# Performance work log

Measured on AMD Instinct MI355X. Metric: run time of the kernel, lower is better.

Reference implementation:

```python
import jax, jax.numpy as jnp
import numpy as np

B, K, N, F, H = 20000, 10, 100000, 256, 128


def setup_inputs() -> dict:
    key = jax.random.key(0)
    ks = jax.random.split(key, 8)
    neighbors = jax.random.randint(ks[0], (B, K), 0, N)
    embed_table = jax.random.normal(ks[1], (N, F), dtype=jnp.float32)
    w = lambda k, shp: jax.random.normal(k, shp, dtype=jnp.float32) * 0.05
    return {
        "neighbors": neighbors,
        "embed_table": embed_table,
        "W1a": w(ks[2], (F, H)), "W1b": w(ks[3], (H, H)),
        "W2a": w(ks[4], (F, H)), "W2b": w(ks[5], (H, H)),
        "W3a": w(ks[6], (F, H)), "W3b": w(ks[7], (H, H)),
    }


def reference(neighbors, embed_table, W1a, W1b, W2a, W2b, W3a, W3b):
    # Gather each batch node's K sampled neighbor embeddings: [B, K, F]
    x = embed_table[neighbors]
    # Three MLP projections: Linear(F,H,no bias) -> tanh -> Linear(H,H,no bias)
    q = jnp.tanh(x @ W1a) @ W1b              # [B, K, H]  (att1)
    k = jnp.tanh(x @ W2a) @ W2b              # [B, K, H]  (att2)
    v = jnp.tanh(x @ W3a) @ W3b              # [B, K, H]  (att3)
    # Per-node attention over the K neighbors, softmax along last dim
    att = jax.nn.softmax(jnp.einsum('bid,bjd->bij', q, k), axis=-1)  # [B, K, K]
    # torch: sum over rows of (att @ v) -> contract both i and j
    out = jnp.einsum('bij,bjd->bd', att, v)  # [B, H]
    return out
```

## Files before the change

### kernel.cpp

```cpp
#include <hip/hip_runtime.h>
#include <hip/hip_bf16.h>

constexpr int B_ = 20000;
constexpr int K_ = 10;
constexpr int N_ = 100000;
constexpr int F_ = 256;
constexpr int H_ = 128;
constexpr int RW = 3 * H_;

typedef __attribute__((ext_vector_type(8))) short bf16x8;
typedef __attribute__((ext_vector_type(4))) float f32x4;
typedef __attribute__((ext_vector_type(4))) unsigned short ushort4v;

__device__ __forceinline__ unsigned short f2bf(float x) {
  unsigned int u = __builtin_bit_cast(unsigned int, x);
  unsigned int r = u + 0x7fffu + ((u >> 16) & 1u);
  return (unsigned short)(r >> 16);
}

__device__ __forceinline__ float bf2f(unsigned int u16) {
  return __builtin_bit_cast(float, u16 << 16);
}

__device__ __forceinline__ unsigned int cvt_pk_bf16(float lo, float hi) {
  unsigned int r;
  asm("v_cvt_pk_bf16_f32 %0, %1, %2" : "=v"(r) : "v"(lo), "v"(hi));
  return r;
}

__device__ __forceinline__ float fast_tanh(float x) {
  float e = __expf(2.0f * x);
  return 1.0f - 2.0f * __builtin_amdgcn_rcpf(e + 1.0f);
}

__global__ __launch_bounds__(256) void prep_kernel(
    const float* __restrict__ W1a, const float* __restrict__ W1b,
    const float* __restrict__ W2a, const float* __restrict__ W2b,
    const float* __restrict__ W3a, const float* __restrict__ W3b,
    unsigned short* __restrict__ wat2, unsigned short* __restrict__ wbt2) {
  const float* Wa[3] = {W1a, W2a, W3a};
  const float* Wb[3] = {W1b, W2b, W3b};
  int g = blockIdx.x * 256 + threadIdx.x;
  if (g < 3 * 64 * 512) {
    int chunk = g >> 9;
    int e = g & 511;
    int lane = e >> 3, j = e & 7;
    int c = chunk & 7;
    int ks = (chunk >> 3) & 7;
    int p = chunk >> 6;
    int k = 32 * ks + 8 * (lane >> 4) + j;
    int h = 16 * c + (lane & 15);
    wat2[g] = f2bf(Wa[p][k * H_ + h]);
  } else {
    int g2 = g - 3 * 64 * 512;
    int chunk = g2 >> 9;
    int e = g2 & 511;
    int lane = e >> 3, j = e & 7;
    int ks2 = chunk & 3;
    int c2 = (chunk >> 2) & 7;
    int p = chunk >> 5;
    int k = 32 * ks2 + 8 * (lane >> 4) + j;
    int h2 = 16 * c2 + (lane & 15);
    wbt2[g2] = f2bf(Wb[p][k * H_ + h2]);
  }
}

constexpr int MT = 32;
constexpr int XS = F_ + 8;
constexpr int TS = H_ + 8;

__global__ __launch_bounds__(256) void proj_kernel(
    const float* __restrict__ E,
    const unsigned short* __restrict__ wat2,
    const unsigned short* __restrict__ wbt2,
    unsigned short* __restrict__ qkvI) {
  __shared__ unsigned short xs[MT * XS];
  __shared__ unsigned short ts[MT * TS];

  const int tid = threadIdx.x;
  const int lane = tid & 63;
  const int w = tid >> 6;
  const int l15 = lane & 15;
  const int q = lane >> 4;
  const int row0 = blockIdx.x * MT;

  {
    const float4* Eg = (const float4*)E;
#pragma unroll
    for (int it = 0; it < 8; ++it) {
      int i = tid + 256 * it;
      int r = i >> 6;
      int c4 = i & 63;
      int row = row0 + r;
      if (row >= N_) row = N_ - 1;
      float4 v = Eg[(size_t)row * (F_ / 4) + c4];
      unsigned int lo = cvt_pk_bf16(v.x, v.y);
      unsigned int hi = cvt_pk_bf16(v.z, v.w);
      *(uint2*)&xs[r * XS + c4 * 4] = make_uint2(lo, hi);
    }
  }
  __syncthreads();

  for (int p = 0; p < 3; ++p) {
    const unsigned short* __restrict__ wa = wat2 + p * (64 * 512);
    const unsigned short* __restrict__ wb = wbt2 + p * (32 * 512);

    bf16x8 af[2][8];
#pragma unroll
    for (int ks = 0; ks < 8; ++ks) {
      af[0][ks] = *(const bf16x8*)&wa[(ks * 8 + 2 * w) * 512 + lane * 8];
      af[1][ks] = *(const bf16x8*)&wa[(ks * 8 + 2 * w + 1) * 512 + lane * 8];
    }

    f32x4 acc[2][2];
#pragma unroll
    for (int i = 0; i < 2; ++i)
#pragma unroll
      for (int j = 0; j < 2; ++j) acc[i][j] = (f32x4)0.0f;

#pragma unroll
    for (int ks = 0; ks < 8; ++ks) {
      bf16x8 bx0 = *(const bf16x8*)&xs[(l15)*XS + 32 * ks + 8 * q];
      bf16x8 bx1 = *(const bf16x8*)&xs[(16 + l15) * XS + 32 * ks + 8 * q];
      acc[0][0] = __builtin_amdgcn_mfma_f32_16x16x32_bf16(af[0][ks], bx0, acc[0][0], 0, 0, 0);
      acc[0][1] = __builtin_amdgcn_mfma_f32_16x16x32_bf16(af[0][ks], bx1, acc[0][1], 0, 0, 0);
      acc[1][0] = __builtin_amdgcn_mfma_f32_16x16x32_bf16(af[1][ks], bx0, acc[1][0], 0, 0, 0);
      acc[1][1] = __builtin_amdgcn_mfma_f32_16x16x32_bf16(af[1][ks], bx1, acc[1][1], 0, 0, 0);
    }

    bf16x8 ab[2][4];
#pragma unroll
    for (int ks2 = 0; ks2 < 4; ++ks2) {
      ab[0][ks2] = *(const bf16x8*)&wb[((2 * w) * 4 + ks2) * 512 + lane * 8];
      ab[1][ks2] = *(const bf16x8*)&wb[((2 * w + 1) * 4 + ks2) * 512 + lane * 8];
    }

    __syncthreads();
#pragma unroll
    for (int i = 0; i < 2; ++i)
#pragma unroll
      for (int j = 0; j < 2; ++j) {
        unsigned int lo = cvt_pk_bf16(fast_tanh(acc[i][j][0]), fast_tanh(acc[i][j][1]));
        unsigned int hi = cvt_pk_bf16(fast_tanh(acc[i][j][2]), fast_tanh(acc[i][j][3]));
        *(uint2*)&ts[(16 * j + l15) * TS + 16 * (2 * w + i) + 4 * q] =
            make_uint2(lo, hi);
      }
    __syncthreads();

    f32x4 ac2[2][2];
#pragma unroll
    for (int i = 0; i < 2; ++i)
#pragma unroll
      for (int j = 0; j < 2; ++j) ac2[i][j] = (f32x4)0.0f;

#pragma unroll
    for (int ks2 = 0; ks2 < 4; ++ks2) {
      bf16x8 bt0 = *(const bf16x8*)&ts[(l15)*TS + 32 * ks2 + 8 * q];
      bf16x8 bt1 = *(const bf16x8*)&ts[(16 + l15) * TS + 32 * ks2 + 8 * q];
      ac2[0][0] = __builtin_amdgcn_mfma_f32_16x16x32_bf16(ab[0][ks2], bt0, ac2[0][0], 0, 0, 0);
      ac2[0][1] = __builtin_amdgcn_mfma_f32_16x16x32_bf16(ab[0][ks2], bt1, ac2[0][1], 0, 0, 0);
      ac2[1][0] = __builtin_amdgcn_mfma_f32_16x16x32_bf16(ab[1][ks2], bt0, ac2[1][0], 0, 0, 0);
      ac2[1][1] = __builtin_amdgcn_mfma_f32_16x16x32_bf16(ab[1][ks2], bt1, ac2[1][1], 0, 0, 0);
    }

#pragma unroll
    for (int i = 0; i < 2; ++i)
#pragma unroll
      for (int j = 0; j < 2; ++j) {
        int n = row0 + 16 * j + l15;
        if (n < N_) {
          unsigned int lo = cvt_pk_bf16(ac2[i][j][0], ac2[i][j][1]);
          unsigned int hi = cvt_pk_bf16(ac2[i][j][2], ac2[i][j][3]);
          *(uint2*)&qkvI[(size_t)n * RW + p * H_ + 16 * (2 * w + i) + 4 * q] =
              make_uint2(lo, hi);
        }
      }
  }
}

__global__ __launch_bounds__(256) void agg_kernel(
    const int* __restrict__ nbr,
    const unsigned short* __restrict__ qkvI,
    float* __restrict__ out) {
  const int lane = threadIdx.x & 63;
  const int wv = threadIdx.x >> 6;
  const int b = blockIdx.x * 4 + wv;
  const int l15 = lane & 15;
  const int kg = lane >> 4;

  const int ni = nbr[b * K_ + (l15 < K_ ? l15 : 0)];
  const size_t nbase = (size_t)ni * RW;

  f32x4 sc = (f32x4)0.0f;
#pragma unroll
  for (int k = 0; k < 4; ++k) {
    const int off = k * 32 + kg * 8;
    bf16x8 qf = *(const bf16x8*)&qkvI[nbase + off];
    bf16x8 kf = *(const bf16x8*)&qkvI[nbase + H_ + off];
    sc = __builtin_amdgcn_mfma_f32_16x16x32_bf16(qf, kf, sc, 0, 0, 0);
  }

  if (l15 >= K_) {
#pragma unroll
    for (int r = 0; r < 4; ++r) sc[r] = -3.0e38f;
  }

  float mx[4], e[4], sm[4];
#pragma unroll
  for (int r = 0; r < 4; ++r) mx[r] = sc[r];
#pragma unroll
  for (int st = 1; st < 16; st <<= 1)
#pragma unroll
    for (int r = 0; r < 4; ++r) mx[r] = fmaxf(mx[r], __shfl_xor(mx[r], st, 16));
#pragma unroll
  for (int r = 0; r < 4; ++r) { e[r] = __expf(sc[r] - mx[r]); sm[r] = e[r]; }
#pragma unroll
  for (int st = 1; st < 16; st <<= 1)
#pragma unroll
    for (int r = 0; r < 4; ++r) sm[r] += __shfl_xor(sm[r], st, 16);

  float cs = 0.0f;
#pragma unroll
  for (int r = 0; r < 4; ++r) {
    float a = e[r] * __builtin_amdgcn_rcpf(sm[r]);
    if (kg * 4 + r >= K_) a = 0.0f;
    cs += a;
  }
  cs += __shfl_xor(cs, 16, 64);
  cs += __shfl_xor(cs, 32, 64);

  float o0 = 0.0f, o1 = 0.0f;
#pragma unroll
  for (int j = 0; j < K_; ++j) {
    const float cj = __shfl(cs, j, 64);
    const int nj = __shfl(ni, j, 64);
    const unsigned int v2 =
        *(const unsigned int*)&qkvI[(size_t)nj * RW + 2 * H_ + 2 * lane];
    o0 = fmaf(cj, bf2f(v2 & 0xffffu), o0);
    o1 = fmaf(cj, bf2f(v2 >> 16), o1);
  }
  *(float2*)&out[(size_t)b * H_ + 2 * lane] = make_float2(o0, o1);
}

extern "C" void kernel_launch(void* const* d_in, const int* in_sizes, int n_in,
                              void* d_out, int out_size, void* d_ws, size_t ws_size,
                              hipStream_t stream) {
  const int* nbr = (const int*)d_in[0];
  const float* E = (const float*)d_in[1];
  const float* W1a = (const float*)d_in[2];
  const float* W1b = (const float*)d_in[3];
  const float* W2a = (const float*)d_in[4];
  const float* W2b = (const float*)d_in[5];
  const float* W3a = (const float*)d_in[6];
  const float* W3b = (const float*)d_in[7];
  float* out = (float*)d_out;

  unsigned short* qkvI = (unsigned short*)d_ws;
  unsigned short* wat2 = qkvI + (size_t)N_ * RW;
  unsigned short* wbt2 = wat2 + (size_t)3 * 64 * 512;

  prep_kernel<<<(3 * 64 * 512 + 3 * 32 * 512) / 256, 256, 0, stream>>>(
      W1a, W1b, W2a, W2b, W3a, W3b, wat2, wbt2);
  proj_kernel<<<N_ / MT, 256, 0, stream>>>(E, wat2, wbt2, qkvI);
  agg_kernel<<<B_ / 4, 256, 0, stream>>>(nbr, qkvI, out);
}
```

Baseline: 236.4 us.

## Double projection row tile to 64 and split warps over H and rows

Measured after the change: 307.7 us. 1.3x slower.

```diff
diff --git a/kernel.cpp b/kernel.cpp
--- a/kernel.cpp
+++ b/kernel.cpp
@@ -10,7 +10,6 @@
 
 typedef __attribute__((ext_vector_type(8))) short bf16x8;
 typedef __attribute__((ext_vector_type(4))) float f32x4;
-typedef __attribute__((ext_vector_type(4))) unsigned short ushort4v;
 
 __device__ __forceinline__ unsigned short f2bf(float x) {
   unsigned int u = __builtin_bit_cast(unsigned int, x);
@@ -65,7 +64,7 @@
   }
 }
 
-constexpr int MT = 32;
+constexpr int MT = 64;
 constexpr int XS = F_ + 8;
 constexpr int TS = H_ + 8;
 
@@ -80,6 +79,8 @@
   const int tid = threadIdx.x;
   const int lane = tid & 63;
   const int w = tid >> 6;
+  const int wh = w >> 1;
+  const int wn = w & 1;
   const int l15 = lane & 15;
   const int q = lane >> 4;
   const int row0 = blockIdx.x * MT;
@@ -87,7 +88,7 @@
   {
     const float4* Eg = (const float4*)E;
 #pragma unroll
-    for (int it = 0; it < 8; ++it) {
+    for (int it = 0; it < 16; ++it) {
       int i = tid + 256 * it;
       int r = i >> 6;
       int c4 = i & 63;
@@ -105,73 +106,63 @@
     const unsigned short* __restrict__ wa = wat2 + p * (64 * 512);
     const unsigned short* __restrict__ wb = wbt2 + p * (32 * 512);
 
-    bf16x8 af[2][8];
+    f32x4 acc[4][2];
+#pragma unroll
+    for (int i = 0; i < 4; ++i)
+#pragma unroll
+      for (int j = 0; j < 2; ++j) acc[i][j] = (f32x4)0.0f;
+
 #pragma unroll
     for (int ks = 0; ks < 8; ++ks) {
-      af[0][ks] = *(const bf16x8*)&wa[(ks * 8 + 2 * w) * 512 + lane * 8];
-      af[1][ks] = *(const bf16x8*)&wa[(ks * 8 + 2 * w + 1) * 512 + lane * 8];
+      bf16x8 bx0 = *(const bf16x8*)&xs[(16 * (2 * wn) + l15) * XS + 32 * ks + 8 * q];
+      bf16x8 bx1 = *(const bf16x8*)&xs[(16 * (2 * wn + 1) + l15) * XS + 32 * ks + 8 * q];
+#pragma unroll
+      for (int i = 0; i < 4; ++i) {
+        bf16x8 af = *(const bf16x8*)&wa[(ks * 8 + 4 * wh + i) * 512 + lane * 8];
+        acc[i][0] = __builtin_amdgcn_mfma_f32_16x16x32_bf16(af, bx0, acc[i][0], 0, 0, 0);
+        acc[i][1] = __builtin_amdgcn_mfma_f32_16x16x32_bf16(af, bx1, acc[i][1], 0, 0, 0);
+      }
     }
 
-    f32x4 acc[2][2];
-#pragma unroll
-    for (int i = 0; i < 2; ++i)
-#pragma unroll
-      for (int j = 0; j < 2; ++j) acc[i][j] = (f32x4)0.0f;
-
-#pragma unroll
-    for (int ks = 0; ks < 8; ++ks) {
-      bf16x8 bx0 = *(const bf16x8*)&xs[(l15)*XS + 32 * ks + 8 * q];
-      bf16x8 bx1 = *(const bf16x8*)&xs[(16 + l15) * XS + 32 * ks + 8 * q];
-      acc[0][0] = __builtin_amdgcn_mfma_f32_16x16x32_bf16(af[0][ks], bx0, acc[0][0], 0, 0, 0);
-      acc[0][1] = __builtin_amdgcn_mfma_f32_16x16x32_bf16(af[0][ks], bx1, acc[0][1], 0, 0, 0);
-      acc[1][0] = __builtin_amdgcn_mfma_f32_16x16x32_bf16(af[1][ks], bx0, acc[1][0], 0, 0, 0);
-      acc[1][1] = __builtin_amdgcn_mfma_f32_16x16x32_bf16(af[1][ks], bx1, acc[1][1], 0, 0, 0);
-    }
-
-    bf16x8 ab[2][4];
-#pragma unroll
-    for (int ks2 = 0; ks2 < 4; ++ks2) {
-      ab[0][ks2] = *(const bf16x8*)&wb[((2 * w) * 4 + ks2) * 512 + lane * 8];
-      ab[1][ks2] = *(const bf16x8*)&wb[((2 * w + 1) * 4 + ks2) * 512 + lane * 8];
-    }
-
     __syncthreads();
 #pragma unroll
-    for (int i = 0; i < 2; ++i)
+    for (int i = 0; i < 4; ++i)
 #pragma unroll
       for (int j = 0; j < 2; ++j) {
         unsigned int lo = cvt_pk_bf16(fast_tanh(acc[i][j][0]), fast_tanh(acc[i][j][1]));
         unsigned int hi = cvt_pk_bf16(fast_tanh(acc[i][j][2]), fast_tanh(acc[i][j][3]));
-        *(uint2*)&ts[(16 * j + l15) * TS + 16 * (2 * w + i) + 4 * q] =
+        *(uint2*)&ts[(16 * (2 * wn + j) + l15) * TS + 16 * (4 * wh + i) + 4 * q] =
             make_uint2(lo, hi);
       }
     __syncthreads();
 
-    f32x4 ac2[2][2];
-#pragma unroll
-    for (int i = 0; i < 2; ++i)
+    f32x4 ac2[4][2];
+#pragma unroll
+    for (int i = 0; i < 4; ++i)
 #pragma unroll
       for (int j = 0; j < 2; ++j) ac2[i][j] = (f32x4)0.0f;
 
 #pragma unroll
     for (int ks2 = 0; ks2 < 4; ++ks2) {
-      bf16x8 bt0 = *(const bf16x8*)&ts[(l15)*TS + 32 * ks2 + 8 * q];
-      bf16x8 bt1 = *(const bf16x8*)&ts[(16 + l15) * TS + 32 * ks2 + 8 * q];
-      ac2[0][0] = __builtin_amdgcn_mfma_f32_16x16x32_bf16(ab[0][ks2], bt0, ac2[0][0], 0, 0, 0);
-      ac2[0][1] = __builtin_amdgcn_mfma_f32_16x16x32_bf16(ab[0][ks2], bt1, ac2[0][1], 0, 0, 0);
-      ac2[1][0] = __builtin_amdgcn_mfma_f32_16x16x32_bf16(ab[1][ks2], bt0, ac2[1][0], 0, 0, 0);
-      ac2[1][1] = __builtin_amdgcn_mfma_f32_16x16x32_bf16(ab[1][ks2], bt1, ac2[1][1], 0, 0, 0);
+      bf16x8 bt0 = *(const bf16x8*)&ts[(16 * (2 * wn) + l15) * TS + 32 * ks2 + 8 * q];
+      bf16x8 bt1 = *(const bf16x8*)&ts[(16 * (2 * wn + 1) + l15) * TS + 32 * ks2 + 8 * q];
+#pragma unroll
+      for (int i = 0; i < 4; ++i) {
+        bf16x8 ab = *(const bf16x8*)&wb[((4 * wh + i) * 4 + ks2) * 512 + lane * 8];
+        ac2[i][0] = __builtin_amdgcn_mfma_f32_16x16x32_bf16(ab, bt0, ac2[i][0], 0, 0, 0);
+        ac2[i][1] = __builtin_amdgcn_mfma_f32_16x16x32_bf16(ab, bt1, ac2[i][1], 0, 0, 0);
+      }
     }
 
 #pragma unroll
-    for (int i = 0; i < 2; ++i)
+    for (int i = 0; i < 4; ++i)
 #pragma unroll
       for (int j = 0; j < 2; ++j) {
-        int n = row0 + 16 * j + l15;
+        int n = row0 + 16 * (2 * wn + j) + l15;
         if (n < N_) {
           unsigned int lo = cvt_pk_bf16(ac2[i][j][0], ac2[i][j][1]);
           unsigned int hi = cvt_pk_bf16(ac2[i][j][2], ac2[i][j][3]);
-          *(uint2*)&qkvI[(size_t)n * RW + p * H_ + 16 * (2 * w + i) + 4 * q] =
+          *(uint2*)&qkvI[(size_t)n * RW + p * H_ + 16 * (4 * wh + i) + 4 * q] =
               make_uint2(lo, hi);
         }
       }
@@ -261,6 +252,6 @@
 
   prep_kernel<<<(3 * 64 * 512 + 3 * 32 * 512) / 256, 256, 0, stream>>>(
       W1a, W1b, W2a, W2b, W3a, W3b, wat2, wbt2);
-  proj_kernel<<<N_ / MT, 256, 0, stream>>>(E, wat2, wbt2, qkvI);
+  proj_kernel<<<(N_ + MT - 1) / MT, 256, 0, stream>>>(E, wat2, wbt2, qkvI);
   agg_kernel<<<B_ / 4, 256, 0, stream>>>(nbr, qkvI, out);
 }
```
